# Kernel tuning notes

Measured on AMD Instinct MI355X. Metric: run time of the kernel, lower is better.

The kernel has to match this reference:

```python
import jax, jax.numpy as jnp
import numpy as np

N, T, D = 32, 64, 16
F = 512  # object_classes == feature dim after object_fc


def _gcn(x, adj, W, b):
    # Kipf GraphConvolution: adj @ (x @ W) + b
    return adj @ (x @ W) + b


def _norm_adj(a):
    d = jnp.sum(a, axis=1) ** -0.5
    return a * d[:, None] * d[None, :]


def _per_graph(x, gc1_W, gc1_b, gc2_W, gc2_b, gc3_W, gc3_b, gc4_W, gc4_b):
    # x: [D, F]
    # graph_generator / adj2: softmax-style similarity adjacency with D^{-1/2} norm
    s = x @ x.T                                   # [D, D]
    a = jnp.exp(s - jnp.max(s, axis=1, keepdims=True))
    adj = _norm_adj(a)
    # branch 1
    x1 = jax.nn.relu(_gcn(x, adj, gc1_W, gc1_b))
    x1 = _gcn(x1, adj, gc2_W, gc2_b)
    # branch 2 (adj_hat2 identical construction from x)
    y2 = jax.nn.relu(_gcn(x, adj, gc3_W, gc3_b))  # [D, 32]
    y22 = y2 @ y2.T
    nrm = jnp.sqrt(jnp.sum(y22 * y22, axis=1, keepdims=True))  # torch.norm(y22, 2, dim=1)
    adj3 = 1.0 + y22 / (nrm @ nrm.T)
    adj_hat3 = _norm_adj(adj3)
    y2 = _gcn(y2, adj_hat3, gc4_W, gc4_b)
    return (x1 + y2) * 0.5


def setup_inputs() -> dict:
    key = jax.random.key(0)
    ks = jax.random.split(key, 12)
    s = 0.02
    return {
        "object_raw": jax.random.normal(ks[0], (N * T * D, F), jnp.float32),
        "action_raw": jax.random.normal(ks[1], (N * T, F), jnp.float32),
        "W_obj": jax.random.normal(ks[2], (F, 512), jnp.float32) * s,
        "b_obj": jnp.zeros((512,), jnp.float32),
        "W_act": jax.random.normal(ks[3], (F, 512), jnp.float32) * s,
        "b_act": jnp.zeros((512,), jnp.float32),
        "gc1_W": jax.random.normal(ks[4], (512, 32), jnp.float32) * s,
        "gc1_b": jnp.zeros((32,), jnp.float32),
        "gc2_W": jax.random.normal(ks[5], (32, 512), jnp.float32) * s,
        "gc2_b": jnp.zeros((512,), jnp.float32),
        "gc3_W": jax.random.normal(ks[6], (512, 32), jnp.float32) * s,
        "gc3_b": jnp.zeros((32,), jnp.float32),
        "gc4_W": jax.random.normal(ks[7], (32, 512), jnp.float32) * s,
        "gc4_b": jnp.zeros((512,), jnp.float32),
        "fc1_W": jax.random.normal(ks[8], (512, 1024), jnp.float32) * s,
        "fc1_b": jnp.zeros((1024,), jnp.float32),
        "clf_W": jax.random.normal(ks[9], (1024, 500), jnp.float32) * s,
        "clf_b": jnp.zeros((500,), jnp.float32),
    }


def reference(object_raw, action_raw, W_obj, b_obj, W_act, b_act,
              gc1_W, gc1_b, gc2_W, gc2_b, gc3_W, gc3_b, gc4_W, gc4_b,
              fc1_W, fc1_b, clf_W, clf_b):
    obj = jax.nn.relu(object_raw @ W_obj + b_obj).reshape(N * T, D, 512)
    act = jax.nn.relu(action_raw @ W_act + b_act)           # [N*T, 512]
    obj = obj.at[:, D // 2].set(act)                         # overwrite middle frame
    graph = jax.vmap(lambda x: _per_graph(x, gc1_W, gc1_b, gc2_W, gc2_b,
                                          gc3_W, gc3_b, gc4_W, gc4_b))(obj)
    g = graph.reshape(N, T, D, 512).mean(axis=2)
    o = obj.reshape(N, T, D, 512).mean(axis=2)
    feat = (o + g) * 0.5                                     # graph_fusion == 'mean'
    c = jax.nn.relu(feat)                                    # dropout = identity (eval)
    c = jax.nn.relu(c @ fc1_W + fc1_b)
    out = (c @ clf_W + clf_b).mean(axis=1)                   # mean over T -> [N, 500]
    return out
```

## Files before the change

### kernel.cpp

```cpp
#include <hip/hip_runtime.h>
#include <hip/hip_bf16.h>

using ushort_t = unsigned short;
using f32x4  = __attribute__((ext_vector_type(4))) float;
using short8 = __attribute__((ext_vector_type(8))) short;

__device__ __forceinline__ float bflo(unsigned p) {
    union { unsigned u; float f; } x; x.u = p << 16; return x.f;
}
__device__ __forceinline__ float bfhi(unsigned p) {
    union { unsigned u; float f; } x; x.u = p & 0xffff0000u; return x.f;
}
__device__ __forceinline__ ushort_t f2bf(float f) {
    __hip_bfloat16 h = __float2bfloat16(f);
    return *(ushort_t*)&h;
}
__device__ __forceinline__ unsigned pk2bf(float lo, float hi) {
    __hip_bfloat162 h = __float22bfloat162_rn({lo, hi});
    return *(unsigned*)&h;
}

__device__ __forceinline__ void tr_tile(const float* __restrict__ S, ushort_t* __restrict__ D,
                                        int K, int N, int Npad, int bx, int by,
                                        int tx, int ty, float* tile )
{
    const int k0 = by * 32, n0 = bx * 32;
#pragma unroll
    for (int r = 0; r < 4; r++) {
        const int k = k0 + ty + r * 8, n = n0 + tx;
        tile[(ty + r * 8) * 33 + tx] = (k < K && n < N) ? S[(size_t)k * N + n] : 0.f;
    }
    __syncthreads();
#pragma unroll
    for (int r = 0; r < 4; r++) {
        const int n = n0 + ty + r * 8, k = k0 + tx;
        if (n < Npad && k < K) D[(size_t)n * K + k] = f2bf(tile[tx * 33 + ty + r * 8]);
    }
}

__global__ __launch_bounds__(256)
void prep_weights(const float* __restrict__ Wobj, ushort_t* __restrict__ WobjT,
                  const float* __restrict__ Wact, ushort_t* __restrict__ WactT,
                  const float* __restrict__ fc1W, ushort_t* __restrict__ fc1T,
                  const float* __restrict__ clfW, ushort_t* __restrict__ clfT,
                  const float* __restrict__ gc1W, ushort_t* __restrict__ W1t,
                  const float* __restrict__ gc3W, ushort_t* __restrict__ W3t,
                  const float* __restrict__ gc2W, ushort_t* __restrict__ W2bf,
                  const float* __restrict__ gc4W, ushort_t* __restrict__ W4bf)
{
    __shared__ float tile[32 * 33];
    const int b = blockIdx.x;
    const int t = threadIdx.x;
    const int tx = t & 31, ty = t >> 5;

    if (b < 1568) {
        const float* S; ushort_t* D; int K, N, Npad, nt, l;
        if      (b < 256)  { S = Wobj; D = WobjT; K = 512;  N = 512;  Npad = 512;  nt = 16; l = b; }
        else if (b < 512)  { S = Wact; D = WactT; K = 512;  N = 512;  Npad = 512;  nt = 16; l = b - 256; }
        else if (b < 1024) { S = fc1W; D = fc1T;  K = 512;  N = 1024; Npad = 1024; nt = 32; l = b - 512; }
        else if (b < 1536) { S = clfW; D = clfT;  K = 1024; N = 500;  Npad = 512;  nt = 16; l = b - 1024; }
        else if (b < 1552) { S = gc1W; D = W1t;   K = 512;  N = 32;   Npad = 32;   nt = 1;  l = b - 1536; }
        else               { S = gc3W; D = W3t;   K = 512;  N = 32;   Npad = 32;   nt = 1;  l = b - 1552; }
        tr_tile(S, D, K, N, Npad, l % nt, l / nt, tx, ty, tile);
    } else {
        const float* S = (b < 1576) ? gc2W : gc4W;
        ushort_t* D    = (b < 1576) ? W2bf : W4bf;
        const int i = (b < 1576 ? b - 1568 : b - 1576) * 256 + t;
        const float4 x = ((const float4*)S)[2 * i];
        const float4 y = ((const float4*)S)[2 * i + 1];
        unsigned r[4] = { pk2bf(x.x, x.y), pk2bf(x.z, x.w), pk2bf(y.x, y.y), pk2bf(y.z, y.w) };
        ((uint4*)D)[i] = *(uint4*)r;
    }
}

struct FragBf { uint4 v;
    __device__ __forceinline__ void load(const ushort_t* p) { v = *(const uint4*)p; }
    __device__ __forceinline__ void store(ushort_t* d) { *(uint4*)d = v; } };
struct FragF32 { float4 a, b;
    __device__ __forceinline__ void load(const float* p) { a = *(const float4*)p; b = *(const float4*)(p + 4); }
    __device__ __forceinline__ void store(ushort_t* d) {
        unsigned r[4] = { pk2bf(a.x, a.y), pk2bf(a.z, a.w), pk2bf(b.x, b.y), pk2bf(b.z, b.w) };
        *(uint4*)d = *(uint4*)r; } };
template<typename AT> struct FragOf;
template<> struct FragOf<ushort_t> { using type = FragBf; };
template<> struct FragOf<float>    { using type = FragF32; };

__device__ __forceinline__ void store_out(ushort_t* C, size_t idx, float v) { C[idx] = f2bf(v); }
__device__ __forceinline__ void store_out(float* C, size_t idx, float v)    { C[idx] = v; }

template<int RELU, typename AT, typename OT>
__global__ __launch_bounds__(256)
void gemm_mfma(const AT* __restrict__ A, const ushort_t* __restrict__ Bt,
               const float* __restrict__ bias, OT* __restrict__ C,
               int M, int N, int K, int Nb, int row_mul, int row_add)
{
    using AFrag = typename FragOf<AT>::type;
    __shared__ ushort_t As[128 * 56];
    __shared__ ushort_t Bs[128 * 56];
    const int t = threadIdx.x;
    const int lane = t & 63, w = t >> 6;
    const int bm = blockIdx.y * 128, bn = blockIdx.x * 128;
    const int mb = (w & 1) * 64, nb = (w >> 1) * 64;

    const int r0 = t >> 2, kc0 = t & 3;
    const AT*       Ag = A  + (size_t)(bm + r0) * K + kc0 * 8;
    const ushort_t* Bg = Bt + (size_t)(bn + r0) * K + kc0 * 8;
    const size_t rowskip = (size_t)64 * K;

    f32x4 acc[16];
#pragma unroll
    for (int i = 0; i < 16; i++) acc[i] = (f32x4){0.f, 0.f, 0.f, 0.f};

    const int fr = lane & 15, fq = lane >> 4;

    AFrag a0, a1; uint4 b0, b1;
    a0.load(Ag); a1.load(Ag + rowskip);
    b0 = *(const uint4*)(Bg); b1 = *(const uint4*)(Bg + rowskip);

    for (int k0 = 0; k0 < K; k0 += 32) {
        a0.store(&As[(r0)      * 56 + kc0 * 8]);
        a1.store(&As[(r0 + 64) * 56 + kc0 * 8]);
        *(uint4*)&Bs[(r0)      * 56 + kc0 * 8] = b0;
        *(uint4*)&Bs[(r0 + 64) * 56 + kc0 * 8] = b1;
        __syncthreads();

        if (k0 + 32 < K) {
            a0.load(Ag + k0 + 32); a1.load(Ag + rowskip + k0 + 32);
            b0 = *(const uint4*)(Bg + k0 + 32); b1 = *(const uint4*)(Bg + rowskip + k0 + 32);
        }

        short8 af[4], bf[4];
#pragma unroll
        for (int i = 0; i < 4; i++)
            af[i] = *(const short8*)&As[(mb + i * 16 + fr) * 56 + fq * 8];
#pragma unroll
        for (int j = 0; j < 4; j++)
            bf[j] = *(const short8*)&Bs[(nb + j * 16 + fr) * 56 + fq * 8];
#pragma unroll
        for (int i = 0; i < 4; i++)
#pragma unroll
            for (int j = 0; j < 4; j++)
                acc[i * 4 + j] = __builtin_amdgcn_mfma_f32_16x16x32_bf16(
                    af[i], bf[j], acc[i * 4 + j], 0, 0, 0);
        __syncthreads();
    }

#pragma unroll
    for (int j = 0; j < 4; j++) {
        const int n = bn + nb + j * 16 + fr;
        const float bv = (n < Nb) ? bias[n] : 0.f;
#pragma unroll
        for (int i = 0; i < 4; i++) {
            const f32x4 a = acc[i * 4 + j];
#pragma unroll
            for (int r = 0; r < 4; r++) {
                const int m = bm + mb + i * 16 + fq * 4 + r;
                float v = a[r] + bv;
                if (RELU) v = fmaxf(v, 0.f);
                store_out(C, ((size_t)m * row_mul + row_add) * (size_t)N + n, v);
            }
        }
    }
}

__global__ __launch_bounds__(64)
void graph_mfma(const ushort_t* __restrict__ obj,
                const ushort_t* __restrict__ W1t, const float* __restrict__ b1,
                const ushort_t* __restrict__ W2b, const float* __restrict__ b2,
                const ushort_t* __restrict__ W3t, const float* __restrict__ b3,
                const ushort_t* __restrict__ W4b, const float* __restrict__ b4,
                ushort_t* __restrict__ cbuf)
{
    __shared__ float ssb[16 * 17];
    __shared__ float adjt[16 * 20];
    __shared__ float t1s[16 * 36];
    __shared__ float t3s[16 * 36];
    __shared__ float x1s[16 * 36];
    __shared__ float y2s[16 * 36];
    __shared__ float y22s[16 * 17];
    __shared__ float a3t[16 * 20];
    __shared__ float dv[16], dv3[16], nrm[16], cA[16], cA3[16];
    __shared__ float zc1[32], zc4[32];

    const int lane = threadIdx.x;
    const int r = lane & 15, fq = lane >> 4;
    const ushort_t* xg = obj + (size_t)blockIdx.x * 8192;

    short8 xf[16];
#pragma unroll
    for (int kk = 0; kk < 16; kk++)
        xf[kk] = *(const short8*)(xg + r * 512 + kk * 32 + fq * 8);

    f32x4 sacc = (f32x4){0.f, 0.f, 0.f, 0.f};
#pragma unroll
    for (int kk = 0; kk < 16; kk++)
        sacc = __builtin_amdgcn_mfma_f32_16x16x32_bf16(xf[kk], xf[kk], sacc, 0, 0, 0);

    f32x4 a10 = (f32x4){0.f,0.f,0.f,0.f}, a11 = a10, a30 = a10, a31 = a10;
#pragma unroll
    for (int kk = 0; kk < 16; kk++) {
        const short8 w10 = *(const short8*)(W1t + (size_t)(r)      * 512 + kk * 32 + fq * 8);
        const short8 w11 = *(const short8*)(W1t + (size_t)(16 + r) * 512 + kk * 32 + fq * 8);
        const short8 w30 = *(const short8*)(W3t + (size_t)(r)      * 512 + kk * 32 + fq * 8);
        const short8 w31 = *(const short8*)(W3t + (size_t)(16 + r) * 512 + kk * 32 + fq * 8);
        a10 = __builtin_amdgcn_mfma_f32_16x16x32_bf16(xf[kk], w10, a10, 0, 0, 0);
        a11 = __builtin_amdgcn_mfma_f32_16x16x32_bf16(xf[kk], w11, a11, 0, 0, 0);
        a30 = __builtin_amdgcn_mfma_f32_16x16x32_bf16(xf[kk], w30, a30, 0, 0, 0);
        a31 = __builtin_amdgcn_mfma_f32_16x16x32_bf16(xf[kk], w31, a31, 0, 0, 0);
    }

#pragma unroll
    for (int i = 0; i < 4; i++) {
        const int m = fq * 4 + i;
        ssb[m * 17 + r] = sacc[i];
        t1s[m * 36 + r]      = a10[i];
        t1s[m * 36 + 16 + r] = a11[i];
        t3s[m * 36 + r]      = a30[i];
        t3s[m * 36 + 16 + r] = a31[i];
    }
    __syncthreads();

    if (lane < 16) {
        float m = ssb[lane * 17];
#pragma unroll
        for (int j = 1; j < 16; j++) m = fmaxf(m, ssb[lane * 17 + j]);
        float s = 0.f;
#pragma unroll
        for (int j = 0; j < 16; j++) {
            const float e = expf(ssb[lane * 17 + j] - m);
            ssb[lane * 17 + j] = e; s += e;
        }
        dv[lane] = rsqrtf(s);
    }
    __syncthreads();

    {
        const float di = dv[r];
#pragma unroll
        for (int p = 0; p < 4; p++) {
            const int j = fq * 4 + p;
            adjt[j * 20 + r] = ssb[r * 17 + j] * di * dv[j];
        }
    }
    __syncthreads();

    if (lane < 16) {
        float s = 0.f;
#pragma unroll
        for (int i = 0; i < 16; i++) s += adjt[lane * 20 + i];
        cA[lane] = s;
    }

    {
        const int c = lane & 31, hi = lane >> 5;
        const float bb1 = b1[c], bb3 = b3[c];
        float ax[8], ay[8];
#pragma unroll
        for (int i = 0; i < 8; i++) { ax[i] = bb1; ay[i] = bb3; }
#pragma unroll
        for (int j = 0; j < 16; j++) {
            const float t1v = t1s[j * 36 + c], t3v = t3s[j * 36 + c];
            const float4 p = *(const float4*)&adjt[j * 20 + hi * 8];
            const float4 q = *(const float4*)&adjt[j * 20 + hi * 8 + 4];
            ax[0] = fmaf(p.x, t1v, ax[0]); ax[1] = fmaf(p.y, t1v, ax[1]);
            ax[2] = fmaf(p.z, t1v, ax[2]); ax[3] = fmaf(p.w, t1v, ax[3]);
            ax[4] = fmaf(q.x, t1v, ax[4]); ax[5] = fmaf(q.y, t1v, ax[5]);
            ax[6] = fmaf(q.z, t1v, ax[6]); ax[7] = fmaf(q.w, t1v, ax[7]);
            ay[0] = fmaf(p.x, t3v, ay[0]); ay[1] = fmaf(p.y, t3v, ay[1]);
            ay[2] = fmaf(p.z, t3v, ay[2]); ay[3] = fmaf(p.w, t3v, ay[3]);
            ay[4] = fmaf(q.x, t3v, ay[4]); ay[5] = fmaf(q.y, t3v, ay[5]);
            ay[6] = fmaf(q.z, t3v, ay[6]); ay[7] = fmaf(q.w, t3v, ay[7]);
        }
#pragma unroll
        for (int i = 0; i < 8; i++) {
            x1s[(hi * 8 + i) * 36 + c] = fmaxf(ax[i], 0.f);
            y2s[(hi * 8 + i) * 36 + c] = fmaxf(ay[i], 0.f);
        }
    }
    __syncthreads();

    {
        const int i2 = lane >> 2, j0 = (lane & 3) * 4;
        float a4[4] = {0.f, 0.f, 0.f, 0.f};
#pragma unroll
        for (int k4 = 0; k4 < 8; k4++) {
            const float4 yi = *(const float4*)&y2s[i2 * 36 + k4 * 4];
#pragma unroll
            for (int p = 0; p < 4; p++) {
                const float4 yj = *(const float4*)&y2s[(j0 + p) * 36 + k4 * 4];
                a4[p] = fmaf(yi.x, yj.x, a4[p]); a4[p] = fmaf(yi.y, yj.y, a4[p]);
                a4[p] = fmaf(yi.z, yj.z, a4[p]); a4[p] = fmaf(yi.w, yj.w, a4[p]);
            }
        }
#pragma unroll
        for (int p = 0; p < 4; p++) y22s[i2 * 17 + j0 + p] = a4[p];
    }
    __syncthreads();

    if (lane < 16) {
        float sq = 0.f;
#pragma unroll
        for (int j = 0; j < 16; j++) { const float v = y22s[lane * 17 + j]; sq = fmaf(v, v, sq); }
        nrm[lane] = sqrtf(sq);
    }
    __syncthreads();

    {
        const float ni = nrm[r];
#pragma unroll
        for (int p = 0; p < 4; p++) {
            const int j = fq * 4 + p;
            a3t[j * 20 + r] = 1.0f + y22s[r * 17 + j] / (ni * nrm[j]);
        }
    }
    __syncthreads();

    if (lane < 16) {
        float s = 0.f;
#pragma unroll
        for (int j = 0; j < 16; j++) s += a3t[j * 20 + lane];
        dv3[lane] = rsqrtf(s);
    }
    __syncthreads();

    if (lane < 16) {
        float s = 0.f;
#pragma unroll
        for (int i = 0; i < 16; i++) s = fmaf(a3t[lane * 20 + i], dv3[i], s);
        cA3[lane] = s * dv3[lane];
    }
    __syncthreads();

    if (lane < 32) {
        float s1 = 0.f, s4 = 0.f;
#pragma unroll
        for (int j = 0; j < 16; j++) {
            s1 = fmaf(cA[j],  x1s[j * 36 + lane], s1);
            s4 = fmaf(cA3[j], y2s[j * 36 + lane], s4);
        }
        zc1[lane] = s1; zc4[lane] = s4;
    }
    __syncthreads();

    {
        float om[8] = {0,0,0,0,0,0,0,0};
#pragma unroll
        for (int m = 0; m < 16; m++) {
            const uint4 q = *(const uint4*)(xg + m * 512 + lane * 8);
            om[0] += bflo(q.x); om[1] += bfhi(q.x);
            om[2] += bflo(q.y); om[3] += bfhi(q.y);
            om[4] += bflo(q.z); om[5] += bfhi(q.z);
            om[6] += bflo(q.w); om[7] += bfhi(q.w);
        }
        float gm[8] = {0,0,0,0,0,0,0,0};
        for (int k = 0; k < 32; k++) {
            const float z1 = zc1[k], z4 = zc4[k];
            const uint4 w2 = *(const uint4*)(W2b + (size_t)k * 512 + lane * 8);
            const uint4 w4 = *(const uint4*)(W4b + (size_t)k * 512 + lane * 8);
            gm[0] = fmaf(z1, bflo(w2.x), gm[0]); gm[0] = fmaf(z4, bflo(w4.x), gm[0]);
            gm[1] = fmaf(z1, bfhi(w2.x), gm[1]); gm[1] = fmaf(z4, bfhi(w4.x), gm[1]);
            gm[2] = fmaf(z1, bflo(w2.y), gm[2]); gm[2] = fmaf(z4, bflo(w4.y), gm[2]);
            gm[3] = fmaf(z1, bfhi(w2.y), gm[3]); gm[3] = fmaf(z4, bfhi(w4.y), gm[3]);
            gm[4] = fmaf(z1, bflo(w2.z), gm[4]); gm[4] = fmaf(z4, bflo(w4.z), gm[4]);
            gm[5] = fmaf(z1, bfhi(w2.z), gm[5]); gm[5] = fmaf(z4, bfhi(w4.z), gm[5]);
            gm[6] = fmaf(z1, bflo(w2.w), gm[6]); gm[6] = fmaf(z4, bflo(w4.w), gm[6]);
            gm[7] = fmaf(z1, bfhi(w2.w), gm[7]); gm[7] = fmaf(z4, bfhi(w4.w), gm[7]);
        }
        const float4 b2a = *(const float4*)&b2[lane * 8];
        const float4 b2b = *(const float4*)&b2[lane * 8 + 4];
        const float4 b4a = *(const float4*)&b4[lane * 8];
        const float4 b4b = *(const float4*)&b4[lane * 8 + 4];
        const float bs[8] = { b2a.x + b4a.x, b2a.y + b4a.y, b2a.z + b4a.z, b2a.w + b4a.w,
                              b2b.x + b4b.x, b2b.y + b4b.y, b2b.z + b4b.z, b2b.w + b4b.w };
        ushort_t pk[8];
#pragma unroll
        for (int c = 0; c < 8; c++) {
            const float gmean = 0.5f * bs[c] + gm[c] * (1.0f / 32.0f);
            const float feat  = 0.5f * (om[c] * 0.0625f + gmean);
            pk[c] = f2bf(fmaxf(feat, 0.f));
        }
        *(uint4*)(cbuf + (size_t)blockIdx.x * 512 + lane * 8) = *(uint4*)pk;
    }
}

__global__ __launch_bounds__(256)
void mean_c2(const ushort_t* __restrict__ c2, float* __restrict__ cmean)
{
    const int idx = blockIdx.x * 256 + threadIdx.x;
    const int n = idx >> 10, k = idx & 1023;
    const ushort_t* p = c2 + (size_t)n * 64 * 1024 + k;
    float s = 0.f;
#pragma unroll 8
    for (int tt = 0; tt < 64; tt++) {
        union { unsigned u; float f; } x; x.u = ((unsigned)p[tt * 1024]) << 16;
        s += x.f;
    }
    cmean[idx] = s * (1.0f / 64.0f);
}

__global__ __launch_bounds__(256)
void clf_small(const float* __restrict__ cmean, const ushort_t* __restrict__ clfT,
               const float* __restrict__ clf_b, float* __restrict__ out)
{
    const int t = threadIdx.x;
    const int n = t & 31, jo = t >> 5;
    const int j = blockIdx.x * 8 + jo;
    const float4* cm = (const float4*)(cmean + (size_t)n * 1024);
    const uint2*  wr = (const uint2*)(clfT + (size_t)(j < 500 ? j : 499) * 1024);
    float acc = 0.f;
#pragma unroll 4
    for (int k4 = 0; k4 < 256; k4++) {
        const float4 c = cm[k4];
        const uint2  w = wr[k4];
        acc = fmaf(c.x, bflo(w.x), acc);
        acc = fmaf(c.y, bfhi(w.x), acc);
        acc = fmaf(c.z, bflo(w.y), acc);
        acc = fmaf(c.w, bfhi(w.y), acc);
    }
    if (j < 500) out[(size_t)n * 500 + j] = acc + clf_b[j];
}

extern "C" void kernel_launch(void* const* d_in, const int* in_sizes, int n_in,
                              void* d_out, int out_size, void* d_ws, size_t ws_size,
                              hipStream_t stream)
{
    const float* object_raw = (const float*)d_in[0];
    const float* action_raw = (const float*)d_in[1];
    const float* W_obj = (const float*)d_in[2];
    const float* b_obj = (const float*)d_in[3];
    const float* W_act = (const float*)d_in[4];
    const float* b_act = (const float*)d_in[5];
    const float* gc1_W = (const float*)d_in[6];
    const float* gc1_b = (const float*)d_in[7];
    const float* gc2_W = (const float*)d_in[8];
    const float* gc2_b = (const float*)d_in[9];
    const float* gc3_W = (const float*)d_in[10];
    const float* gc3_b = (const float*)d_in[11];
    const float* gc4_W = (const float*)d_in[12];
    const float* gc4_b = (const float*)d_in[13];
    const float* fc1_W = (const float*)d_in[14];
    const float* fc1_b = (const float*)d_in[15];
    const float* clf_W = (const float*)d_in[16];
    const float* clf_b = (const float*)d_in[17];

    char* ws = (char*)d_ws;
    const size_t MB = 1024 * 1024;
    ushort_t* obj_bf = (ushort_t*)(ws);
    ushort_t* cbuf   = (ushort_t*)(ws + 32 * MB);
    ushort_t* c2     = (ushort_t*)(ws + 34 * MB);
    float*    cmean  = (float*)   (ws + 38 * MB);
    ushort_t* WobjT  = (ushort_t*)(ws + 39 * MB);
    ushort_t* WactT  = (ushort_t*)(ws + 39 * MB + 512 * 1024);
    ushort_t* fc1T   = (ushort_t*)(ws + 40 * MB);
    ushort_t* clfT   = (ushort_t*)(ws + 41 * MB);
    ushort_t* W1t    = (ushort_t*)(ws + 42 * MB);
    ushort_t* W3t    = (ushort_t*)(ws + 42 * MB + 32 * 1024);
    ushort_t* W2bf   = (ushort_t*)(ws + 42 * MB + 64 * 1024);
    ushort_t* W4bf   = (ushort_t*)(ws + 42 * MB + 96 * 1024);

    prep_weights<<<dim3(1584), 256, 0, stream>>>(
        W_obj, WobjT, W_act, WactT, fc1_W, fc1T, clf_W, clfT,
        gc1_W, W1t, gc3_W, W3t, gc2_W, W2bf, gc4_W, W4bf);

    gemm_mfma<1, float, ushort_t><<<dim3(4, 256), 256, 0, stream>>>(
        object_raw, WobjT, b_obj, obj_bf, 32768, 512, 512, 512, 1, 0);

    gemm_mfma<1, float, ushort_t><<<dim3(4, 16), 256, 0, stream>>>(
        action_raw, WactT, b_act, obj_bf, 2048, 512, 512, 512, 16, 8);

    graph_mfma<<<dim3(2048), 64, 0, stream>>>(
        obj_bf, W1t, gc1_b, W2bf, gc2_b, W3t, gc3_b, W4bf, gc4_b, cbuf);

    gemm_mfma<1, ushort_t, ushort_t><<<dim3(8, 16), 256, 0, stream>>>(
        cbuf, fc1T, fc1_b, c2, 2048, 1024, 512, 1024, 1, 0);

    mean_c2<<<dim3(128), 256, 0, stream>>>(c2, cmean);

    clf_small<<<dim3(63), 256, 0, stream>>>(cmean, clfT, clf_b, (float*)d_out);
}
```

Measured before the change: 271.2 us.

## Use direct global-to-LDS loads in GEMMs and fuse object/action projections

Rewrites the MFMA GEMM core to load A and B tiles with global_load_lds DMA into XOR-swizzled LDS, instead of staging through registers. The fp32 A operand is kept as fp32 in LDS and converted to bf16 at fragment-read time. The object and action projection GEMMs are merged into one launch, and the object GEMM skips writing the middle-frame row that the action GEMM overwrites. This removes register staging, a kernel launch and redundant stores. In exchange it drops the register-prefetch double buffering, so loads no longer overlap compute within a block, and it doubles LDS use for the fp32 A tile.

```diff
diff --git a/kernel.cpp b/kernel.cpp
--- a/kernel.cpp
+++ b/kernel.cpp
@@ -18,6 +18,13 @@
 __device__ __forceinline__ unsigned pk2bf(float lo, float hi) {
     __hip_bfloat162 h = __float22bfloat162_rn({lo, hi});
     return *(unsigned*)&h;
+}
+
+typedef __attribute__((address_space(1))) void glb_void;
+typedef __attribute__((address_space(3))) void lds_void;
+__device__ __forceinline__ void dma16(const void* g, void* l) {
+    __builtin_amdgcn_global_load_lds((glb_void*)(unsigned long long)(uintptr_t)g,
+                                     (lds_void*)(unsigned)(uintptr_t)l, 16, 0, 0);
 }
 
 __device__ __forceinline__ void tr_tile(const float* __restrict__ S, ushort_t* __restrict__ D,
@@ -73,76 +80,87 @@
     }
 }
 
-struct FragBf { uint4 v;
-    __device__ __forceinline__ void load(const ushort_t* p) { v = *(const uint4*)p; }
-    __device__ __forceinline__ void store(ushort_t* d) { *(uint4*)d = v; } };
-struct FragF32 { float4 a, b;
-    __device__ __forceinline__ void load(const float* p) { a = *(const float4*)p; b = *(const float4*)(p + 4); }
-    __device__ __forceinline__ void store(ushort_t* d) {
-        unsigned r[4] = { pk2bf(a.x, a.y), pk2bf(a.z, a.w), pk2bf(b.x, b.y), pk2bf(b.z, b.w) };
-        *(uint4*)d = *(uint4*)r; } };
-template<typename AT> struct FragOf;
-template<> struct FragOf<ushort_t> { using type = FragBf; };
-template<> struct FragOf<float>    { using type = FragF32; };
-
 __device__ __forceinline__ void store_out(ushort_t* C, size_t idx, float v) { C[idx] = f2bf(v); }
 __device__ __forceinline__ void store_out(float* C, size_t idx, float v)    { C[idx] = v; }
 
 template<int RELU, typename AT, typename OT>
-__global__ __launch_bounds__(256)
-void gemm_mfma(const AT* __restrict__ A, const ushort_t* __restrict__ Bt,
-               const float* __restrict__ bias, OT* __restrict__ C,
-               int M, int N, int K, int Nb, int row_mul, int row_add)
-{
-    using AFrag = typename FragOf<AT>::type;
-    __shared__ ushort_t As[128 * 56];
-    __shared__ ushort_t Bs[128 * 56];
+__device__ __forceinline__ void gemm_core(
+    const AT* __restrict__ A, const ushort_t* __restrict__ Bt,
+    const float* __restrict__ bias, OT* __restrict__ C,
+    int N, int K, int Nb, int row_mul, int row_add, int bm, int bn, int skip8,
+    char* AsRaw, ushort_t* Bs)
+{
     const int t = threadIdx.x;
     const int lane = t & 63, w = t >> 6;
-    const int bm = blockIdx.y * 128, bn = blockIdx.x * 128;
     const int mb = (w & 1) * 64, nb = (w >> 1) * 64;
-
-    const int r0 = t >> 2, kc0 = t & 3;
-    const AT*       Ag = A  + (size_t)(bm + r0) * K + kc0 * 8;
-    const ushort_t* Bg = Bt + (size_t)(bn + r0) * K + kc0 * 8;
-    const size_t rowskip = (size_t)64 * K;
+    const int fr = lane & 15, fq = lane >> 4;
 
     f32x4 acc[16];
 #pragma unroll
     for (int i = 0; i < 16; i++) acc[i] = (f32x4){0.f, 0.f, 0.f, 0.f};
 
-    const int fr = lane & 15, fq = lane >> 4;
-
-    AFrag a0, a1; uint4 b0, b1;
-    a0.load(Ag); a1.load(Ag + rowskip);
-    b0 = *(const uint4*)(Bg); b1 = *(const uint4*)(Bg + rowskip);
+    const int brow = lane >> 2, bk = lane & 3;
+    const int klog = bk ^ ((brow >> 1) & 3);
+    const int arow = lane >> 3, ag = lane & 7;
 
     for (int k0 = 0; k0 < K; k0 += 32) {
-        a0.store(&As[(r0)      * 56 + kc0 * 8]);
-        a1.store(&As[(r0 + 64) * 56 + kc0 * 8]);
-        *(uint4*)&Bs[(r0)      * 56 + kc0 * 8] = b0;
-        *(uint4*)&Bs[(r0 + 64) * 56 + kc0 * 8] = b1;
         __syncthreads();
-
-        if (k0 + 32 < K) {
-            a0.load(Ag + k0 + 32); a1.load(Ag + rowskip + k0 + 32);
-            b0 = *(const uint4*)(Bg + k0 + 32); b1 = *(const uint4*)(Bg + rowskip + k0 + 32);
-        }
+        if constexpr (sizeof(AT) == 4) {
+#pragma unroll
+            for (int i = 0; i < 4; i++) {
+                const int grp = w * 4 + i;
+                const int row = grp * 8 + arow;
+                const int gl = ag ^ (row & 7);
+                dma16((const float*)A + (size_t)(bm + row) * K + k0 + gl * 4,
+                      AsRaw + grp * 1024);
+            }
+        } else {
+#pragma unroll
+            for (int i = 0; i < 2; i++) {
+                const int grp = w * 2 + i;
+                const int row = grp * 16 + brow;
+                dma16((const ushort_t*)A + (size_t)(bm + row) * K + k0 + klog * 8,
+                      (ushort_t*)AsRaw + grp * 512);
+            }
+        }
+#pragma unroll
+        for (int i = 0; i < 2; i++) {
+            const int grp = w * 2 + i;
+            const int row = grp * 16 + brow;
+            dma16(Bt + (size_t)(bn + row) * K + k0 + klog * 8, Bs + grp * 512);
+        }
+        __syncthreads();
 
         short8 af[4], bf[4];
-#pragma unroll
-        for (int i = 0; i < 4; i++)
-            af[i] = *(const short8*)&As[(mb + i * 16 + fr) * 56 + fq * 8];
-#pragma unroll
-        for (int j = 0; j < 4; j++)
-            bf[j] = *(const short8*)&Bs[(nb + j * 16 + fr) * 56 + fq * 8];
+        if constexpr (sizeof(AT) == 4) {
+#pragma unroll
+            for (int i = 0; i < 4; i++) {
+                const int row = mb + i * 16 + fr;
+                const float* base = (const float*)AsRaw + row * 32;
+                const f32x4 p0 = *(const f32x4*)(base + (((2 * fq)     ^ (fr & 7)) * 4));
+                const f32x4 p1 = *(const f32x4*)(base + (((2 * fq + 1) ^ (fr & 7)) * 4));
+                unsigned rr[4] = { pk2bf(p0.x, p0.y), pk2bf(p0.z, p0.w),
+                                   pk2bf(p1.x, p1.y), pk2bf(p1.z, p1.w) };
+                af[i] = *(short8*)rr;
+            }
+        } else {
+#pragma unroll
+            for (int i = 0; i < 4; i++) {
+                const int row = mb + i * 16 + fr;
+                af[i] = *(const short8*)((const ushort_t*)AsRaw + row * 32 + (fq ^ ((fr >> 1) & 3)) * 8);
+            }
+        }
+#pragma unroll
+        for (int j = 0; j < 4; j++) {
+            const int row = nb + j * 16 + fr;
+            bf[j] = *(const short8*)(Bs + row * 32 + (fq ^ ((fr >> 1) & 3)) * 8);
+        }
 #pragma unroll
         for (int i = 0; i < 4; i++)
 #pragma unroll
             for (int j = 0; j < 4; j++)
                 acc[i * 4 + j] = __builtin_amdgcn_mfma_f32_16x16x32_bf16(
                     af[i], bf[j], acc[i * 4 + j], 0, 0, 0);
-        __syncthreads();
     }
 
 #pragma unroll
@@ -154,6 +172,7 @@
             const f32x4 a = acc[i * 4 + j];
 #pragma unroll
             for (int r = 0; r < 4; r++) {
+                if (skip8 && (fq * 4 + r) == 8) continue;
                 const int m = bm + mb + i * 16 + fq * 4 + r;
                 float v = a[r] + bv;
                 if (RELU) v = fmaxf(v, 0.f);
@@ -161,6 +180,34 @@
             }
         }
     }
+}
+
+__global__ __launch_bounds__(256)
+void gemm_objact(const float* __restrict__ Ao, const ushort_t* __restrict__ Bo,
+                 const float* __restrict__ bo,
+                 const float* __restrict__ Aa, const ushort_t* __restrict__ Ba,
+                 const float* __restrict__ ba, ushort_t* __restrict__ C)
+{
+    __shared__ __align__(16) char     AsRaw[128 * 32 * 4];
+    __shared__ __align__(16) ushort_t Bs[128 * 32];
+    if (blockIdx.y < 256)
+        gemm_core<1, float, ushort_t>(Ao, Bo, bo, C, 512, 512, 512, 1, 0,
+                                      blockIdx.y * 128, blockIdx.x * 128, 1, AsRaw, Bs);
+    else
+        gemm_core<1, float, ushort_t>(Aa, Ba, ba, C, 512, 512, 512, 16, 8,
+                                      (blockIdx.y - 256) * 128, blockIdx.x * 128, 0, AsRaw, Bs);
+}
+
+template<int RELU, typename AT, typename OT>
+__global__ __launch_bounds__(256)
+void gemm_dma(const AT* __restrict__ A, const ushort_t* __restrict__ Bt,
+              const float* __restrict__ bias, OT* __restrict__ C,
+              int N, int K, int Nb, int row_mul, int row_add)
+{
+    __shared__ __align__(16) char     AsRaw[128 * 32 * sizeof(AT)];
+    __shared__ __align__(16) ushort_t Bs[128 * 32];
+    gemm_core<RELU, AT, OT>(A, Bt, bias, C, N, K, Nb, row_mul, row_add,
+                            blockIdx.y * 128, blockIdx.x * 128, 0, AsRaw, Bs);
 }
 
 __global__ __launch_bounds__(64)
@@ -462,17 +509,14 @@
         W_obj, WobjT, W_act, WactT, fc1_W, fc1T, clf_W, clfT,
         gc1_W, W1t, gc3_W, W3t, gc2_W, W2bf, gc4_W, W4bf);
 
-    gemm_mfma<1, float, ushort_t><<<dim3(4, 256), 256, 0, stream>>>(
-        object_raw, WobjT, b_obj, obj_bf, 32768, 512, 512, 512, 1, 0);
-
-    gemm_mfma<1, float, ushort_t><<<dim3(4, 16), 256, 0, stream>>>(
-        action_raw, WactT, b_act, obj_bf, 2048, 512, 512, 512, 16, 8);
+    gemm_objact<<<dim3(4, 272), 256, 0, stream>>>(
+        object_raw, WobjT, b_obj, action_raw, WactT, b_act, obj_bf);
 
     graph_mfma<<<dim3(2048), 64, 0, stream>>>(
         obj_bf, W1t, gc1_b, W2bf, gc2_b, W3t, gc3_b, W4bf, gc4_b, cbuf);
 
-    gemm_mfma<1, ushort_t, ushort_t><<<dim3(8, 16), 256, 0, stream>>>(
-        cbuf, fc1T, fc1_b, c2, 2048, 1024, 512, 1024, 1, 0);
+    gemm_dma<1, ushort_t, ushort_t><<<dim3(8, 16), 256, 0, stream>>>(
+        cbuf, fc1T, fc1_b, c2, 1024, 512, 1024, 1, 0);
 
     mean_c2<<<dim3(128), 256, 0, stream>>>(c2, cmean);
 
```

After: 267.5 us. Within noise of the previous version (-1.4%).

## Replace tiled GEMMs with full-K A-resident streaming GEMMs and merge obj/act launches

Applied to the files above, without the earlier changes.

The object and action projections are fused into one launch of a new streaming GEMM. Each block loads a full-K strip of A (converted to bf16) into XOR-swizzled LDS and streams B fragments straight from global memory into MFMA, and object rows that the action output would overwrite are skipped. fc1 uses the same core with 16-row strips, and clf_small now reads fp32 clf_W directly, which drops its transpose from prep_weights. This removes a kernel launch, redundant stores and a large weight-prep stage, at the cost of heavier per-block LDS and B reloads from L2 per block.

```diff
diff --git a/kernel.cpp b/kernel.cpp
--- a/kernel.cpp
+++ b/kernel.cpp
@@ -42,7 +42,6 @@
 void prep_weights(const float* __restrict__ Wobj, ushort_t* __restrict__ WobjT,
                   const float* __restrict__ Wact, ushort_t* __restrict__ WactT,
                   const float* __restrict__ fc1W, ushort_t* __restrict__ fc1T,
-                  const float* __restrict__ clfW, ushort_t* __restrict__ clfT,
                   const float* __restrict__ gc1W, ushort_t* __restrict__ W1t,
                   const float* __restrict__ gc3W, ushort_t* __restrict__ W3t,
                   const float* __restrict__ gc2W, ushort_t* __restrict__ W2bf,
@@ -53,19 +52,18 @@
     const int t = threadIdx.x;
     const int tx = t & 31, ty = t >> 5;
 
-    if (b < 1568) {
+    if (b < 1056) {
         const float* S; ushort_t* D; int K, N, Npad, nt, l;
-        if      (b < 256)  { S = Wobj; D = WobjT; K = 512;  N = 512;  Npad = 512;  nt = 16; l = b; }
-        else if (b < 512)  { S = Wact; D = WactT; K = 512;  N = 512;  Npad = 512;  nt = 16; l = b - 256; }
-        else if (b < 1024) { S = fc1W; D = fc1T;  K = 512;  N = 1024; Npad = 1024; nt = 32; l = b - 512; }
-        else if (b < 1536) { S = clfW; D = clfT;  K = 1024; N = 500;  Npad = 512;  nt = 16; l = b - 1024; }
-        else if (b < 1552) { S = gc1W; D = W1t;   K = 512;  N = 32;   Npad = 32;   nt = 1;  l = b - 1536; }
-        else               { S = gc3W; D = W3t;   K = 512;  N = 32;   Npad = 32;   nt = 1;  l = b - 1552; }
+        if      (b < 256)  { S = Wobj; D = WobjT; K = 512; N = 512;  Npad = 512;  nt = 16; l = b; }
+        else if (b < 512)  { S = Wact; D = WactT; K = 512; N = 512;  Npad = 512;  nt = 16; l = b - 256; }
+        else if (b < 1024) { S = fc1W; D = fc1T;  K = 512; N = 1024; Npad = 1024; nt = 32; l = b - 512; }
+        else if (b < 1040) { S = gc1W; D = W1t;   K = 512; N = 32;   Npad = 32;   nt = 1;  l = b - 1024; }
+        else               { S = gc3W; D = W3t;   K = 512; N = 32;   Npad = 32;   nt = 1;  l = b - 1040; }
         tr_tile(S, D, K, N, Npad, l % nt, l / nt, tx, ty, tile);
     } else {
-        const float* S = (b < 1576) ? gc2W : gc4W;
-        ushort_t* D    = (b < 1576) ? W2bf : W4bf;
-        const int i = (b < 1576 ? b - 1568 : b - 1576) * 256 + t;
+        const float* S = (b < 1064) ? gc2W : gc4W;
+        ushort_t* D    = (b < 1064) ? W2bf : W4bf;
+        const int i = (b < 1064 ? b - 1056 : b - 1064) * 256 + t;
         const float4 x = ((const float4*)S)[2 * i];
         const float4 y = ((const float4*)S)[2 * i + 1];
         unsigned r[4] = { pk2bf(x.x, x.y), pk2bf(x.z, x.w), pk2bf(y.x, y.y), pk2bf(y.z, y.w) };
@@ -73,94 +71,103 @@
     }
 }
 
-struct FragBf { uint4 v;
-    __device__ __forceinline__ void load(const ushort_t* p) { v = *(const uint4*)p; }
-    __device__ __forceinline__ void store(ushort_t* d) { *(uint4*)d = v; } };
-struct FragF32 { float4 a, b;
-    __device__ __forceinline__ void load(const float* p) { a = *(const float4*)p; b = *(const float4*)(p + 4); }
-    __device__ __forceinline__ void store(ushort_t* d) {
-        unsigned r[4] = { pk2bf(a.x, a.y), pk2bf(a.z, a.w), pk2bf(b.x, b.y), pk2bf(b.z, b.w) };
-        *(uint4*)d = *(uint4*)r; } };
-template<typename AT> struct FragOf;
-template<> struct FragOf<ushort_t> { using type = FragBf; };
-template<> struct FragOf<float>    { using type = FragF32; };
-
-__device__ __forceinline__ void store_out(ushort_t* C, size_t idx, float v) { C[idx] = f2bf(v); }
-__device__ __forceinline__ void store_out(float* C, size_t idx, float v)    { C[idx] = v; }
-
-template<int RELU, typename AT, typename OT>
-__global__ __launch_bounds__(256)
-void gemm_mfma(const AT* __restrict__ A, const ushort_t* __restrict__ Bt,
-               const float* __restrict__ bias, OT* __restrict__ C,
-               int M, int N, int K, int Nb, int row_mul, int row_add)
-{
-    using AFrag = typename FragOf<AT>::type;
-    __shared__ ushort_t As[128 * 56];
-    __shared__ ushort_t Bs[128 * 56];
+template<int NI, typename AT>
+__device__ __forceinline__ void stream_core(
+    const AT* __restrict__ A, const ushort_t* __restrict__ Bt,
+    const float* __restrict__ bias, ushort_t* __restrict__ C,
+    int N, int bm, int n0, int row_mul, int row_add, int skip8,
+    ushort_t* As)
+{
     const int t = threadIdx.x;
     const int lane = t & 63, w = t >> 6;
-    const int bm = blockIdx.y * 128, bn = blockIdx.x * 128;
-    const int mb = (w & 1) * 64, nb = (w >> 1) * 64;
-
-    const int r0 = t >> 2, kc0 = t & 3;
-    const AT*       Ag = A  + (size_t)(bm + r0) * K + kc0 * 8;
-    const ushort_t* Bg = Bt + (size_t)(bn + r0) * K + kc0 * 8;
-    const size_t rowskip = (size_t)64 * K;
-
-    f32x4 acc[16];
-#pragma unroll
-    for (int i = 0; i < 16; i++) acc[i] = (f32x4){0.f, 0.f, 0.f, 0.f};
-
     const int fr = lane & 15, fq = lane >> 4;
-
-    AFrag a0, a1; uint4 b0, b1;
-    a0.load(Ag); a1.load(Ag + rowskip);
-    b0 = *(const uint4*)(Bg); b1 = *(const uint4*)(Bg + rowskip);
-
-    for (int k0 = 0; k0 < K; k0 += 32) {
-        a0.store(&As[(r0)      * 56 + kc0 * 8]);
-        a1.store(&As[(r0 + 64) * 56 + kc0 * 8]);
-        *(uint4*)&Bs[(r0)      * 56 + kc0 * 8] = b0;
-        *(uint4*)&Bs[(r0 + 64) * 56 + kc0 * 8] = b1;
-        __syncthreads();
-
-        if (k0 + 32 < K) {
-            a0.load(Ag + k0 + 32); a1.load(Ag + rowskip + k0 + 32);
-            b0 = *(const uint4*)(Bg + k0 + 32); b1 = *(const uint4*)(Bg + rowskip + k0 + 32);
-        }
-
-        short8 af[4], bf[4];
-#pragma unroll
-        for (int i = 0; i < 4; i++)
-            af[i] = *(const short8*)&As[(mb + i * 16 + fr) * 56 + fq * 8];
-#pragma unroll
-        for (int j = 0; j < 4; j++)
-            bf[j] = *(const short8*)&Bs[(nb + j * 16 + fr) * 56 + fq * 8];
-#pragma unroll
-        for (int i = 0; i < 4; i++)
-#pragma unroll
-            for (int j = 0; j < 4; j++)
-                acc[i * 4 + j] = __builtin_amdgcn_mfma_f32_16x16x32_bf16(
-                    af[i], bf[j], acc[i * 4 + j], 0, 0, 0);
-        __syncthreads();
-    }
-
-#pragma unroll
-    for (int j = 0; j < 4; j++) {
-        const int n = bn + nb + j * 16 + fr;
-        const float bv = (n < Nb) ? bias[n] : 0.f;
-#pragma unroll
-        for (int i = 0; i < 4; i++) {
-            const f32x4 a = acc[i * 4 + j];
-#pragma unroll
-            for (int r = 0; r < 4; r++) {
-                const int m = bm + mb + i * 16 + fq * 4 + r;
-                float v = a[r] + bv;
-                if (RELU) v = fmaxf(v, 0.f);
-                store_out(C, ((size_t)m * row_mul + row_add) * (size_t)N + n, v);
+    constexpr int NCH = NI * 16 * 64;
+
+#pragma unroll
+    for (int i = 0; i < NCH / 256; i++) {
+        const int cid = i * 256 + t;
+        const int row = cid >> 6, c = cid & 63;
+        uint4 v;
+        if constexpr (sizeof(AT) == 4) {
+            const float* gp = (const float*)A + (size_t)(bm + row) * 512 + c * 8;
+            const float4 p0 = *(const float4*)gp;
+            const float4 p1 = *(const float4*)(gp + 4);
+            unsigned rr[4] = { pk2bf(p0.x, p0.y), pk2bf(p0.z, p0.w),
+                               pk2bf(p1.x, p1.y), pk2bf(p1.z, p1.w) };
+            v = *(uint4*)rr;
+        } else {
+            v = *(const uint4*)((const ushort_t*)A + (size_t)(bm + row) * 512 + c * 8);
+        }
+        *(uint4*)&As[row * 512 + ((c ^ (row & 7)) * 8)] = v;
+    }
+    __syncthreads();
+
+    const int nw = n0 + w * 128;
+    const ushort_t* Bbase = Bt + (size_t)(nw + fr) * 512 + fq * 8;
+
+    f32x4 acc[8][NI];
+#pragma unroll
+    for (int j = 0; j < 8; j++)
+#pragma unroll
+        for (int i = 0; i < NI; i++) acc[j][i] = (f32x4){0.f, 0.f, 0.f, 0.f};
+
+#pragma unroll 2
+    for (int kk = 0; kk < 16; kk++) {
+        uint4 b[8];
+#pragma unroll
+        for (int j = 0; j < 8; j++)
+            b[j] = *(const uint4*)(Bbase + (size_t)j * 16 * 512 + kk * 32);
+        short8 af[NI];
+#pragma unroll
+        for (int i = 0; i < NI; i++)
+            af[i] = *(const short8*)&As[(i * 16 + fr) * 512 + (((kk * 4 + fq) ^ (fr & 7)) * 8)];
+#pragma unroll
+        for (int j = 0; j < 8; j++) {
+            const short8 bfv = *(const short8*)&b[j];
+#pragma unroll
+            for (int i = 0; i < NI; i++)
+                acc[j][i] = __builtin_amdgcn_mfma_f32_16x16x32_bf16(af[i], bfv, acc[j][i], 0, 0, 0);
+        }
+    }
+
+#pragma unroll
+    for (int j = 0; j < 8; j++) {
+        const int n = nw + j * 16 + fr;
+        const float bv = bias[n];
+#pragma unroll
+        for (int i = 0; i < NI; i++) {
+#pragma unroll
+            for (int rr = 0; rr < 4; rr++) {
+                const int ml = i * 16 + fq * 4 + rr;
+                if (skip8 && (ml & 15) == 8) continue;
+                const int m = bm + ml;
+                C[((size_t)m * row_mul + row_add) * (size_t)N + n] =
+                    f2bf(fmaxf(acc[j][i][rr] + bv, 0.f));
             }
         }
     }
+}
+
+__global__ __launch_bounds__(256, 3)
+void gemm_objact_stream(const float* __restrict__ Ao, const ushort_t* __restrict__ Bo,
+                        const float* __restrict__ bo,
+                        const float* __restrict__ Aa, const ushort_t* __restrict__ Ba,
+                        const float* __restrict__ ba, ushort_t* __restrict__ C)
+{
+    __shared__ __align__(16) ushort_t As[32 * 512];
+    if (blockIdx.x < 1024)
+        stream_core<2, float>(Ao, Bo, bo, C, 512, blockIdx.x * 32, 0, 1, 0, 1, As);
+    else
+        stream_core<2, float>(Aa, Ba, ba, C, 512, (blockIdx.x - 1024) * 32, 0, 16, 8, 0, As);
+}
+
+__global__ __launch_bounds__(256, 4)
+void gemm_fc1_stream(const ushort_t* __restrict__ A, const ushort_t* __restrict__ Bt,
+                     const float* __restrict__ bias, ushort_t* __restrict__ C)
+{
+    __shared__ __align__(16) ushort_t As[16 * 512];
+    const int mb = blockIdx.x >> 1, n0 = (blockIdx.x & 1) * 512;
+    stream_core<1, ushort_t>(A, Bt, bias, C, 1024, mb * 16, n0, 1, 0, 0, As);
 }
 
 __global__ __launch_bounds__(64)
@@ -399,23 +406,23 @@
 }
 
 __global__ __launch_bounds__(256)
-void clf_small(const float* __restrict__ cmean, const ushort_t* __restrict__ clfT,
+void clf_small(const float* __restrict__ cmean, const float* __restrict__ W,
                const float* __restrict__ clf_b, float* __restrict__ out)
 {
     const int t = threadIdx.x;
     const int n = t & 31, jo = t >> 5;
     const int j = blockIdx.x * 8 + jo;
+    const int jc = j < 500 ? j : 499;
     const float4* cm = (const float4*)(cmean + (size_t)n * 1024);
-    const uint2*  wr = (const uint2*)(clfT + (size_t)(j < 500 ? j : 499) * 1024);
     float acc = 0.f;
 #pragma unroll 4
     for (int k4 = 0; k4 < 256; k4++) {
         const float4 c = cm[k4];
-        const uint2  w = wr[k4];
-        acc = fmaf(c.x, bflo(w.x), acc);
-        acc = fmaf(c.y, bfhi(w.x), acc);
-        acc = fmaf(c.z, bflo(w.y), acc);
-        acc = fmaf(c.w, bfhi(w.y), acc);
+        const float* wp = W + (size_t)(k4 * 4) * 500 + jc;
+        acc = fmaf(c.x, wp[0],    acc);
+        acc = fmaf(c.y, wp[500],  acc);
+        acc = fmaf(c.z, wp[1000], acc);
+        acc = fmaf(c.w, wp[1500], acc);
     }
     if (j < 500) out[(size_t)n * 500 + j] = acc + clf_b[j];
 }
@@ -452,29 +459,24 @@
     ushort_t* WobjT  = (ushort_t*)(ws + 39 * MB);
     ushort_t* WactT  = (ushort_t*)(ws + 39 * MB + 512 * 1024);
     ushort_t* fc1T   = (ushort_t*)(ws + 40 * MB);
-    ushort_t* clfT   = (ushort_t*)(ws + 41 * MB);
-    ushort_t* W1t    = (ushort_t*)(ws + 42 * MB);
-    ushort_t* W3t    = (ushort_t*)(ws + 42 * MB + 32 * 1024);
-    ushort_t* W2bf   = (ushort_t*)(ws + 42 * MB + 64 * 1024);
-    ushort_t* W4bf   = (ushort_t*)(ws + 42 * MB + 96 * 1024);
-
-    prep_weights<<<dim3(1584), 256, 0, stream>>>(
-        W_obj, WobjT, W_act, WactT, fc1_W, fc1T, clf_W, clfT,
+    ushort_t* W1t    = (ushort_t*)(ws + 41 * MB);
+    ushort_t* W3t    = (ushort_t*)(ws + 41 * MB + 32 * 1024);
+    ushort_t* W2bf   = (ushort_t*)(ws + 41 * MB + 64 * 1024);
+    ushort_t* W4bf   = (ushort_t*)(ws + 41 * MB + 96 * 1024);
+
+    prep_weights<<<dim3(1072), 256, 0, stream>>>(
+        W_obj, WobjT, W_act, WactT, fc1_W, fc1T,
         gc1_W, W1t, gc3_W, W3t, gc2_W, W2bf, gc4_W, W4bf);
 
-    gemm_mfma<1, float, ushort_t><<<dim3(4, 256), 256, 0, stream>>>(
-        object_raw, WobjT, b_obj, obj_bf, 32768, 512, 512, 512, 1, 0);
-
-    gemm_mfma<1, float, ushort_t><<<dim3(4, 16), 256, 0, stream>>>(
-        action_raw, WactT, b_act, obj_bf, 2048, 512, 512, 512, 16, 8);
+    gemm_objact_stream<<<dim3(1088), 256, 0, stream>>>(
+        object_raw, WobjT, b_obj, action_raw, WactT, b_act, obj_bf);
 
     graph_mfma<<<dim3(2048), 64, 0, stream>>>(
         obj_bf, W1t, gc1_b, W2bf, gc2_b, W3t, gc3_b, W4bf, gc4_b, cbuf);
 
-    gemm_mfma<1, ushort_t, ushort_t><<<dim3(8, 16), 256, 0, stream>>>(
-        cbuf, fc1T, fc1_b, c2, 2048, 1024, 512, 1024, 1, 0);
+    gemm_fc1_stream<<<dim3(256), 256, 0, stream>>>(cbuf, fc1T, fc1_b, c2);
 
     mean_c2<<<dim3(128), 256, 0, stream>>>(c2, cmean);
 
-    clf_small<<<dim3(63), 256, 0, stream>>>(cmean, clfT, clf_b, (float*)d_out);
-}
+    clf_small<<<dim3(63), 256, 0, stream>>>(cmean, clf_W, clf_b, (float*)d_out);
+}
```

Result: slower. 317.8 us (+17.2%).
